# Performance work log

Measured on AMD Instinct MI355X. Metric: run time of the kernel, lower is better.

The kernel has to match this reference:

```python
import jax, jax.numpy as jnp
import numpy as np

N = 50_000        # nodes
E = 1_600_000     # edges (avg degree 32)
H = 64            # hidden_channels
DEPTH = 3         # -> 2*DEPTH mid conv layers


def setup_inputs() -> dict:
    key = jax.random.key(0)
    ks = jax.random.split(key, 8)
    x = jax.random.normal(ks[0], (N, 1), dtype=jnp.float32)
    edge_index = jax.random.randint(ks[1], (2, E), 0, N, dtype=jnp.int32)
    s = 0.1  # small init scale
    W_in = s * jax.random.normal(ks[2], (2 * 1 + 1, H), dtype=jnp.float32)
    b_in = jnp.zeros((H,), jnp.float32)
    W_mid = s * jax.random.normal(ks[3], (2 * DEPTH, 2 * H + 1, H), dtype=jnp.float32)
    b_mid = jnp.zeros((2 * DEPTH, H), jnp.float32)
    W_out = s * jax.random.normal(ks[4], (2 * H + 1, 1), dtype=jnp.float32)
    b_out = jnp.zeros((1,), jnp.float32)
    return {"x": x, "edge_index": edge_index, "W_in": W_in, "b_in": b_in,
            "W_mid": W_mid, "b_mid": b_mid, "W_out": W_out, "b_out": b_out}


def _conv(x, src, dst, sign, inv_deg, W, b):
    """Directional_EdgeConv: mean_{j->i} Linear([x_i, x_j - x_i, sign(j-i)])."""
    x_i = x[dst]                                   # [E, F] target feats
    x_j = x[src]                                   # [E, F] source feats
    feat = jnp.concatenate([x_i, x_j - x_i, sign], axis=-1)  # [E, 2F+1]
    msg = feat @ W + b                             # [E, out]
    agg = jax.ops.segment_sum(msg, dst, num_segments=x.shape[0])  # [N, out]
    return agg * inv_deg                           # mean aggregation


def reference(x, edge_index, W_in, b_in, W_mid, b_mid, W_out, b_out):
    src = edge_index[0]
    dst = edge_index[1]
    # vectorized replacement of the per-edge Python sign loop
    sign = jnp.sign((src - dst).astype(x.dtype))[:, None]        # [E, 1]
    deg = jax.ops.segment_sum(jnp.ones((src.shape[0],), x.dtype), dst,
                              num_segments=x.shape[0])
    inv_deg = (1.0 / jnp.maximum(deg, 1.0))[:, None]             # [N, 1]

    x2 = _conv(x, src, dst, sign, inv_deg, W_in, b_in)
    for l in range(DEPTH):
        x1 = jax.nn.leaky_relu(
            _conv(x2, src, dst, sign, inv_deg, W_mid[2 * l], b_mid[2 * l]))
        x2 = jax.nn.leaky_relu(
            _conv(x1, src, dst, sign, inv_deg, W_mid[2 * l + 1], b_mid[2 * l + 1]) + x2)
    return _conv(x2, src, dst, sign, inv_deg, W_out, b_out) + x
```

## Files before the change

kernel.cpp:

```cpp
#include <hip/hip_runtime.h>
#include <hip/hip_fp16.h>

#define HDIM 64
#define NEG_SLOPE 0.01f
#define CAPB 8192
#define BCAP 6144
#define EPB  4096

typedef _Float16 half8 __attribute__((ext_vector_type(8)));
typedef float f32x4 __attribute__((ext_vector_type(4)));

static __device__ __forceinline__ float h_lo(unsigned d) {
    return __half2float(__ushort_as_half((unsigned short)(d & 0xffffu)));
}
static __device__ __forceinline__ float h_hi(unsigned d) {
    return __half2float(__ushort_as_half((unsigned short)(d >> 16)));
}
static __device__ __forceinline__ unsigned packh(float a, float b) {
    unsigned short ra = __half_as_ushort(__float2half(a));
    unsigned short rb = __half_as_ushort(__float2half(b));
    return ((unsigned)rb << 16) | (unsigned)ra;
}
static __device__ __forceinline__ half8 u4h(uint4 v) {
    union { uint4 u; half8 h; } x; x.u = v; return x.h;
}
static __device__ __forceinline__ __half2 uh2(unsigned u) {
    union { unsigned u; __half2 h; } x; x.u = u; return x.h;
}

__global__ void k_setup(int ptotal, const float* __restrict__ W_mid,
                        unsigned short* __restrict__ WTh,
                        int NB, int* gcur, int N, unsigned* xAP, unsigned* xBP,
                        float* tvec) {
    int i = blockIdx.x * blockDim.x + threadIdx.x;
    if (i < ptotal) {
        int l = i >> 13;
        int rem = i & 8191;
        int h = rem >> 7;
        int k = rem & 127;
        const float* W = W_mid + (size_t)l * 129 * 64;
        float v = W[k * 64 + h] - ((k < 64) ? W[(64 + k) * 64 + h] : 0.f);
        WTh[i] = __half_as_ushort(__float2half(v));
    }
    if (i < NB) gcur[i] = i * CAPB;
    if (i < 32) xAP[(size_t)N * 32 + i] = 0u;
    else if (i < 64) xBP[(size_t)N * 32 + (i - 32)] = 0u;
    else if (i == 64) tvec[N] = 0.f;
}

__global__ __launch_bounds__(1024) void k_bucket(
        int E, const int* __restrict__ src, const int* __restrict__ dst,
        int* gcur, unsigned* __restrict__ bucketed, int NB) {
    __shared__ int lh[512];
    __shared__ int sd[512];
    __shared__ int lbase[512];
    __shared__ unsigned sorted[EPB];
    int t = threadIdx.x;
    int e0 = blockIdx.x * EPB;
    if (t < 512) lh[t] = 0;
    __syncthreads();
    int dv[4], sv[4], rv[4];
#pragma unroll
    for (int k = 0; k < 4; ++k) {
        int e = e0 + k * 1024 + t;
        dv[k] = (e < E) ? dst[e] : -1;
        sv[k] = (e < E) ? src[e] : 0;
    }
#pragma unroll
    for (int k = 0; k < 4; ++k)
        rv[k] = (dv[k] >= 0) ? atomicAdd(&lh[((unsigned)dv[k]) >> 7], 1) : 0;
    __syncthreads();
    int c = (t < 512) ? lh[t] : 0;
    if (t < 512) {
        lbase[t] = (c > 0) ? atomicAdd(&gcur[t], c) : 0;
        sd[t] = c;
    }
    __syncthreads();
    int x = c;
    for (int s = 1; s < 512; s <<= 1) {
        int p = (t < 512 && t >= s) ? sd[t - s] : 0;
        __syncthreads();
        if (t < 512) { x += p; sd[t] = x; }
        __syncthreads();
    }
#pragma unroll
    for (int k = 0; k < 4; ++k) {
        if (dv[k] >= 0) {
            int b = ((unsigned)dv[k]) >> 7;
            sorted[sd[b] - lh[b] + rv[k]] = ((unsigned)dv[k] << 16) | (unsigned)sv[k];
        }
    }
    __syncthreads();
    int ntot = sd[511];
    for (int i = t; i < ntot; i += 1024) {
        unsigned w = sorted[i];
        int b = (int)(w >> 23);
        int pos = lbase[b] + (i - (sd[b] - lh[b]));
        if (pos < (b + 1) * CAPB) bucketed[pos] = w;
    }
}

__global__ __launch_bounds__(512) void k_csr(
        int N, int NB, const unsigned* __restrict__ bucketed, const int* __restrict__ gcur,
        unsigned short* __restrict__ csr, unsigned short* __restrict__ pcsr,
        int* __restrict__ rowptr, float* __restrict__ ssinv,
        const float* __restrict__ x0, const float* __restrict__ W_in,
        const float* __restrict__ b_in, unsigned* __restrict__ xAP) {
    __shared__ unsigned st[BCAP];
    __shared__ unsigned short lpcsr[128 * 64];
    __shared__ int hist[128], cur[128], excl[128], sgp[128], sdegl[128];
    __shared__ float sssl[128];
    __shared__ int gsd[512];
    int b = blockIdx.x, t = threadIdx.x;
    int n0 = b << 7;
    int nn = min(128, N - n0);
    int cc = (t < NB) ? min(gcur[t] - t * CAPB, CAPB) : 0;
    gsd[t] = cc;
    __syncthreads();
    int xs = cc;
    for (int s = 1; s < 512; s <<= 1) {
        int p = (t >= s) ? gsd[t - s] : 0;
        __syncthreads();
        xs += p;
        gsd[t] = xs;
        __syncthreads();
    }
    int cnt = min(gcur[b] - b * CAPB, CAPB);
    int base = gsd[b] - cnt;
    if (b == NB - 1 && t == 0) rowptr[N] = gsd[NB - 1];
    if (t < 128) { hist[t] = 0; sgp[t] = 0; }
    unsigned sent = ((unsigned)N << 16) | (unsigned)N;
    for (int i = t; i < 4096; i += 512) ((unsigned*)lpcsr)[i] = sent;
    __syncthreads();
    bool single = (cnt <= BCAP);
    for (int off = 0; off < cnt; off += BCAP) {
        int bs = min(BCAP, cnt - off);
        for (int i = t; i < bs; i += 512) {
            unsigned w = bucketed[b * CAPB + off + i];
            if (single) st[i] = w;
            int d = (int)(w >> 16);
            int s = (int)(w & 0xffffu);
            int dl = d - n0;
            atomicAdd(&hist[dl], 1);
            atomicAdd(&sgp[dl], ((s < d) ? 1024 : 0) + ((s == d) ? 1 : 0));
        }
    }
    __syncthreads();
    int deg_t = (t < 128) ? hist[t] : 0;
    int x = deg_t;
    for (int s = 1; s < 128; s <<= 1) {
        int p = (t < 128 && t >= s) ? hist[t - s] : 0;
        __syncthreads();
        if (t < 128) { x += p; hist[t] = x; }
        __syncthreads();
    }
    if (t < 128) {
        int ex = hist[t] - deg_t;
        excl[t] = ex;
        cur[t] = ex;
        sdegl[t] = deg_t;
        float ssv = 0.f;
        if (t < nn) {
            rowptr[n0 + t] = base + ex;
            int sg = sgp[t];
            int lt = sg >> 10, eq = sg & 1023;
            float ss = (float)(deg_t - eq - 2 * lt);
            ssv = (deg_t > 0) ? ss / (float)deg_t : 0.f;
            ssinv[n0 + t] = ssv;
        }
        sssl[t] = ssv;
    }
    __syncthreads();
    for (int off = 0; off < cnt; off += BCAP) {
        int bs = min(BCAP, cnt - off);
        if (!single) {
            for (int i = t; i < bs; i += 512) st[i] = bucketed[b * CAPB + off + i];
            __syncthreads();
        }
        for (int i = t; i < bs; i += 512) {
            unsigned w = st[i];
            int dl = (int)(w >> 16) - n0;
            unsigned short sval = (unsigned short)(w & 0xffffu);
            int p = atomicAdd(&cur[dl], 1);
            csr[base + p] = sval;
            int r = p - excl[dl];
            if (r < 64) lpcsr[(dl << 6) + r] = sval;
        }
        if (!single) __syncthreads();
    }
    __syncthreads();
    {
        uint4* gp = (uint4*)(pcsr + ((size_t)b << 13));
        const uint4* lp = (const uint4*)lpcsr;
        for (int i = t; i < 1024; i += 512) gp[i] = lp[i];
    }
    int lane = t & 63;
    int wvq = t >> 6;
    float w1 = W_in[lane], w2 = W_in[64 + lane], w3 = W_in[128 + lane];
    float bi = b_in[lane];
    for (int i = 0; i < 16; ++i) {
        int nd = (wvq << 4) + i;
        int node = n0 + nd;
        if (node >= N) break;
        int deg = sdegl[nd];
        float s;
        if (deg <= 64) {
            int sl = (int)lpcsr[(nd << 6) + lane];
            s = (sl < N) ? x0[sl] : 0.f;
        } else {
            s = 0.f;
            int bg = base + excl[nd], en = bg + deg;
            for (int e = bg + lane; e < en; e += 64) s += x0[csr[e]];
        }
        for (int m = 32; m >= 1; m >>= 1) s += __shfl_xor(s, m, 64);
        float invd = 1.f / (float)max(deg, 1);
        float mean = s * invd;
        float xi = x0[node];
        float y = xi * (w1 - w2) + mean * w2 + sssl[nd] * w3 + bi;
        if (deg == 0) y = 0.f;
        float ylo = __shfl(y, (2 * lane) & 63, 64);
        float yhi = __shfl(y, (2 * lane + 1) & 63, 64);
        if (lane < 32) xAP[(size_t)node * 32 + lane] = packh(ylo, yhi);
    }
}

static __device__ __forceinline__ void chunk_acc(
        const uint4* __restrict__ xin16, int sv, int base, int sub, int lq,
        __half2& c0, __half2& c1, __half2& c2, __half2& c3) {
    int s0 = __shfl(sv, base + sub, 64);
    int s1 = __shfl(sv, base + 8 + sub, 64);
    int s2 = __shfl(sv, base + 16 + sub, 64);
    int s3 = __shfl(sv, base + 24 + sub, 64);
    uint4 d0 = xin16[(size_t)s0 * 8 + lq];
    uint4 d1 = xin16[(size_t)s1 * 8 + lq];
    uint4 d2 = xin16[(size_t)s2 * 8 + lq];
    uint4 d3 = xin16[(size_t)s3 * 8 + lq];
    c0 = __hadd2(c0, __hadd2(__hadd2(uh2(d0.x), uh2(d1.x)), __hadd2(uh2(d2.x), uh2(d3.x))));
    c1 = __hadd2(c1, __hadd2(__hadd2(uh2(d0.y), uh2(d1.y)), __hadd2(uh2(d2.y), uh2(d3.y))));
    c2 = __hadd2(c2, __hadd2(__hadd2(uh2(d0.z), uh2(d1.z)), __hadd2(uh2(d2.z), uh2(d3.z))));
    c3 = __hadd2(c3, __hadd2(__hadd2(uh2(d0.w), uh2(d1.w)), __hadd2(uh2(d2.w), uh2(d3.w))));
}

static __device__ __forceinline__ void slow_gather(
        const uint4* __restrict__ xin16, const unsigned short* __restrict__ csr,
        int beg, int end, int N, int lane, int sub, int lq, float* a) {
#pragma unroll
    for (int j = 0; j < 8; ++j) a[j] = 0.f;
    for (int tb = beg; tb < end; tb += 64) {
        int cnt = min(64, end - tb);
        int sv = (lane < cnt) ? (int)csr[tb + lane] : N;
        int ng = (cnt + 7) >> 3;
        for (int g = 0; g < ng; ++g) {
            int si = __shfl(sv, (g << 3) + sub, 64);
            uint4 d = xin16[(size_t)si * 8 + lq];
            a[0] += h_lo(d.x); a[1] += h_hi(d.x);
            a[2] += h_lo(d.y); a[3] += h_hi(d.y);
            a[4] += h_lo(d.z); a[5] += h_hi(d.z);
            a[6] += h_lo(d.w); a[7] += h_hi(d.w);
        }
    }
#pragma unroll
    for (int m = 8; m <= 32; m <<= 1) {
#pragma unroll
        for (int j = 0; j < 8; ++j) a[j] += __shfl_xor(a[j], m, 64);
    }
}

template <bool RES, bool TOUT>
__global__ __launch_bounds__(256) void k_layer(
        int N, const unsigned* __restrict__ xinP,
        const unsigned* __restrict__ xresP, unsigned* __restrict__ xoutP,
        const int* __restrict__ rowptr, const unsigned short* __restrict__ csr,
        const unsigned short* __restrict__ pcsr,
        const float* __restrict__ ssinv,
        const unsigned short* __restrict__ WThl,
        const float* __restrict__ W3, const float* __restrict__ bias,
        const float* __restrict__ Wt, float* __restrict__ tvec) {
    __shared__ unsigned Ald[16 * 64];
    __shared__ float Cld[16 * 64];
    __shared__ int sdeg[16];
    __shared__ float sss[16];

    int t = threadIdx.x;
    int lane = t & 63;
    int wv = t >> 6;
    int n0 = blockIdx.x << 4;
    int kg = lane >> 4;

    int cb = (wv << 4) + (lane & 15);
    const uint4* wp = (const uint4*)WThl;
    uint4 b0 = wp[cb * 16 + kg + 0];
    uint4 b1 = wp[cb * 16 + kg + 4];
    uint4 b2 = wp[cb * 16 + kg + 8];
    uint4 b3 = wp[cb * 16 + kg + 12];

    const uint4* xin16 = (const uint4*)xinP;
    int sub = lane >> 3;
    int lq = lane & 7;
    int ndb = wv << 2;

    int svp[4];
#pragma unroll
    for (int q = 0; q < 4; ++q)
        svp[q] = (int)pcsr[((size_t)(n0 + ndb + q) << 6) + lane];

#pragma unroll
    for (int qp = 0; qp < 2; ++qp) {
        int ndA = ndb + (qp << 1);
        int ndB = ndA + 1;
        int nodeA = n0 + ndA, nodeB = n0 + ndB;
        int ncA = min(nodeA, N - 1), ncB = min(nodeB, N - 1);
        int begA = __builtin_amdgcn_readfirstlane(rowptr[ncA]);
        int endA = __builtin_amdgcn_readfirstlane(rowptr[ncA + 1]);
        int begB = __builtin_amdgcn_readfirstlane(rowptr[ncB]);
        int endB = __builtin_amdgcn_readfirstlane(rowptr[ncB + 1]);
        int degA = (nodeA < N) ? (endA - begA) : 0;
        int degB = (nodeB < N) ? (endB - begB) : 0;
        float ssvA = ssinv[ncA];
        float ssvB = ssinv[ncB];
        uint4 xiA = make_uint4(0u, 0u, 0u, 0u), xiB = make_uint4(0u, 0u, 0u, 0u);
        if (lane < 8) {
            if (nodeA < N) xiA = xin16[(size_t)ncA * 8 + lane];
            if (nodeB < N) xiB = xin16[(size_t)ncB * 8 + lane];
        }
        uint4 mvA, mvB;
        if (max(degA, degB) <= 64) {
            __half2 z = uh2(0u);
            __half2 cA0 = z, cA1 = z, cA2 = z, cA3 = z;
            __half2 cB0 = z, cB1 = z, cB2 = z, cB3 = z;
            int svA = svp[qp << 1], svB = svp[(qp << 1) + 1];
            chunk_acc(xin16, svA, 0, sub, lq, cA0, cA1, cA2, cA3);
            chunk_acc(xin16, svB, 0, sub, lq, cB0, cB1, cB2, cB3);
            if (degA > 32) chunk_acc(xin16, svA, 32, sub, lq, cA0, cA1, cA2, cA3);
            if (degB > 32) chunk_acc(xin16, svB, 32, sub, lq, cB0, cB1, cB2, cB3);
#pragma unroll
            for (int m = 8; m <= 32; m <<= 1) {
                cA0 = __hadd2(cA0, uh2((unsigned)__shfl_xor((int)*(unsigned*)&cA0, m, 64)));
                cA1 = __hadd2(cA1, uh2((unsigned)__shfl_xor((int)*(unsigned*)&cA1, m, 64)));
                cA2 = __hadd2(cA2, uh2((unsigned)__shfl_xor((int)*(unsigned*)&cA2, m, 64)));
                cA3 = __hadd2(cA3, uh2((unsigned)__shfl_xor((int)*(unsigned*)&cA3, m, 64)));
                cB0 = __hadd2(cB0, uh2((unsigned)__shfl_xor((int)*(unsigned*)&cB0, m, 64)));
                cB1 = __hadd2(cB1, uh2((unsigned)__shfl_xor((int)*(unsigned*)&cB1, m, 64)));
                cB2 = __hadd2(cB2, uh2((unsigned)__shfl_xor((int)*(unsigned*)&cB2, m, 64)));
                cB3 = __hadd2(cB3, uh2((unsigned)__shfl_xor((int)*(unsigned*)&cB3, m, 64)));
            }
            float idA = 1.f / (float)max(degA, 1);
            float idB = 1.f / (float)max(degB, 1);
            mvA.x = packh(__half2float(__low2half(cA0)) * idA, __half2float(__high2half(cA0)) * idA);
            mvA.y = packh(__half2float(__low2half(cA1)) * idA, __half2float(__high2half(cA1)) * idA);
            mvA.z = packh(__half2float(__low2half(cA2)) * idA, __half2float(__high2half(cA2)) * idA);
            mvA.w = packh(__half2float(__low2half(cA3)) * idA, __half2float(__high2half(cA3)) * idA);
            mvB.x = packh(__half2float(__low2half(cB0)) * idB, __half2float(__high2half(cB0)) * idB);
            mvB.y = packh(__half2float(__low2half(cB1)) * idB, __half2float(__high2half(cB1)) * idB);
            mvB.z = packh(__half2float(__low2half(cB2)) * idB, __half2float(__high2half(cB2)) * idB);
            mvB.w = packh(__half2float(__low2half(cB3)) * idB, __half2float(__high2half(cB3)) * idB);
        } else {
            float aA[8], aB[8];
            slow_gather(xin16, csr, begA, endA, N, lane, sub, lq, aA);
            slow_gather(xin16, csr, begB, endB, N, lane, sub, lq, aB);
            float idA = 1.f / (float)max(degA, 1);
            float idB = 1.f / (float)max(degB, 1);
            mvA.x = packh(aA[0] * idA, aA[1] * idA);
            mvA.y = packh(aA[2] * idA, aA[3] * idA);
            mvA.z = packh(aA[4] * idA, aA[5] * idA);
            mvA.w = packh(aA[6] * idA, aA[7] * idA);
            mvB.x = packh(aB[0] * idB, aB[1] * idB);
            mvB.y = packh(aB[2] * idB, aB[3] * idB);
            mvB.z = packh(aB[4] * idB, aB[5] * idB);
            mvB.w = packh(aB[6] * idB, aB[7] * idB);
        }
        if (lane < 8) {
            int gxA = lane ^ (ndA & 7), gmA = (8 + lane) ^ (ndA & 7);
            int gxB = lane ^ (ndB & 7), gmB = (8 + lane) ^ (ndB & 7);
            ((uint4*)Ald)[ndA * 16 + gxA] = xiA;
            ((uint4*)Ald)[ndA * 16 + gmA] = mvA;
            ((uint4*)Ald)[ndB * 16 + gxB] = xiB;
            ((uint4*)Ald)[ndB * 16 + gmB] = mvB;
        }
        if (lane == 0) {
            sdeg[ndA] = degA; sss[ndA] = ssvA;
            sdeg[ndB] = degB; sss[ndB] = ssvB;
        }
    }
    __syncthreads();

    int r = lane & 15;
    const uint4* ap = (const uint4*)Ald;
    int rx = (r & 7);
    uint4 fa0 = ap[r * 16 + ((0 + kg) ^ rx)];
    uint4 fa1 = ap[r * 16 + ((4 + kg) ^ rx)];
    uint4 fa2 = ap[r * 16 + ((8 + kg) ^ rx)];
    uint4 fa3 = ap[r * 16 + ((12 + kg) ^ rx)];
    f32x4 acc = {0.f, 0.f, 0.f, 0.f};
    acc = __builtin_amdgcn_mfma_f32_16x16x32_f16(u4h(fa0), u4h(b0), acc, 0, 0, 0);
    acc = __builtin_amdgcn_mfma_f32_16x16x32_f16(u4h(fa1), u4h(b1), acc, 0, 0, 0);
    acc = __builtin_amdgcn_mfma_f32_16x16x32_f16(u4h(fa2), u4h(b2), acc, 0, 0, 0);
    acc = __builtin_amdgcn_mfma_f32_16x16x32_f16(u4h(fa3), u4h(b3), acc, 0, 0, 0);
#pragma unroll
    for (int reg = 0; reg < 4; ++reg)
        Cld[(kg * 4 + reg) * 64 + (wv << 4) + r] = acc[reg];
    __syncthreads();

    int nd = t >> 4;
    int node = n0 + nd;
    if (node < N) {
        int dg = sdeg[nd];
        float ss = sss[nd];
        float tp = 0.f;
#pragma unroll
        for (int jj = 0; jj < 2; ++jj) {
            int j = (t & 15) + jj * 16;
            float y0 = Cld[nd * 64 + 2 * j];
            float y1 = Cld[nd * 64 + 2 * j + 1];
            float2 w3 = ((const float2*)W3)[j];
            float2 bb = ((const float2*)bias)[j];
            y0 += ss * w3.x + bb.x;
            y1 += ss * w3.y + bb.y;
            if (dg == 0) { y0 = 0.f; y1 = 0.f; }
            if (RES) {
                unsigned rw = xresP[(size_t)node * 32 + j];
                y0 += h_lo(rw);
                y1 += h_hi(rw);
            }
            y0 = (y0 > 0.f) ? y0 : NEG_SLOPE * y0;
            y1 = (y1 > 0.f) ? y1 : NEG_SLOPE * y1;
            if (TOUT) {
                float2 wt = ((const float2*)Wt)[j];
                tp += y0 * wt.x + y1 * wt.y;
            }
            xoutP[(size_t)node * 32 + j] = packh(y0, y1);
        }
        if (TOUT) {
            tp += __shfl_xor(tp, 1, 64);
            tp += __shfl_xor(tp, 2, 64);
            tp += __shfl_xor(tp, 4, 64);
            tp += __shfl_xor(tp, 8, 64);
            if ((t & 15) == 0) tvec[node] = tp;
        }
    }
}

__global__ void k_out(int N, const unsigned* __restrict__ xAP, const float* __restrict__ x0,
                      const int* __restrict__ rowptr, const unsigned short* __restrict__ csr,
                      const unsigned short* __restrict__ pcsr,
                      const float* __restrict__ ssinv, const float* __restrict__ t,
                      const float* __restrict__ W_out, const float* __restrict__ b_out,
                      float* __restrict__ out) {
    int wid = blockIdx.x * (blockDim.x >> 6) + (threadIdx.x >> 6);
    int lane = threadIdx.x & 63;
    if (wid >= N) return;
    int beg = rowptr[wid], end = rowptr[wid + 1];
    int deg = end - beg;
    float s;
    if (deg <= 64) {
        int sl = (int)pcsr[((size_t)wid << 6) + lane];
        s = t[sl];
    } else {
        s = 0.f;
        for (int e = beg + lane; e < end; e += 64) s += t[csr[e]];
    }
    unsigned xw = xAP[(size_t)wid * 32 + (lane >> 1)];
    float xf = (lane & 1) ? h_hi(xw) : h_lo(xw);
    float p = xf * (W_out[lane] - W_out[64 + lane]);
    for (int m = 32; m >= 1; m >>= 1) {
        s += __shfl_xor(s, m, 64);
        p += __shfl_xor(p, m, 64);
    }
    float invd = 1.f / (float)max(deg, 1);
    float y = p + s * invd + ssinv[wid] * W_out[128] + b_out[0];
    if (deg == 0) y = 0.f;
    if (lane == 0) out[wid] = y + x0[wid];
}

static inline size_t align16(size_t x) { return (x + 15) & ~(size_t)15; }

extern "C" void kernel_launch(void* const* d_in, const int* in_sizes, int n_in,
                              void* d_out, int out_size, void* d_ws, size_t ws_size,
                              hipStream_t stream) {
    const float* x0    = (const float*)d_in[0];
    const int*   ei    = (const int*)d_in[1];
    const float* W_in  = (const float*)d_in[2];
    const float* b_in  = (const float*)d_in[3];
    const float* W_mid = (const float*)d_in[4];
    const float* b_mid = (const float*)d_in[5];
    const float* W_out = (const float*)d_in[6];
    const float* b_out = (const float*)d_in[7];
    float* out = (float*)d_out;

    const int N = in_sizes[0];
    const int E = in_sizes[1] / 2;
    const int L = in_sizes[4] / (129 * 64);
    const int NB = (N + 127) >> 7;
    const int* src = ei;
    const int* dst = ei + E;

    char* p = (char*)d_ws;
    unsigned short* WTh = (unsigned short*)p; p += align16((size_t)L * 64 * 128 * 2);
    unsigned* xAP = (unsigned*)p; p += align16((size_t)(N + 1) * 32 * 4);
    unsigned* xBP = (unsigned*)p; p += align16((size_t)(N + 1) * 32 * 4);
    unsigned* bucketed = (unsigned*)p; p += align16((size_t)NB * CAPB * 4);
    unsigned short* csr = (unsigned short*)p; p += align16((size_t)E * 2);
    unsigned short* pcsr = (unsigned short*)p; p += align16((size_t)NB * 8192 * 2);
    int* gcur          = (int*)p; p += align16((size_t)(NB + 1) * 4);
    int* rowptr        = (int*)p; p += align16((size_t)(N + 1) * 4);
    float* ssinv       = (float*)p; p += align16((size_t)N * 4);
    float* t           = (float*)p; p += align16((size_t)(N + 1) * 4);

    const int nb_w4 = (N + 3) / 4;
    const int nb_bkt = (E + EPB - 1) / EPB;
    const int ptotal = L * 64 * 128;
    const int nb_lay = (N + 15) / 16;

    k_setup<<<(ptotal + 255) / 256, 256, 0, stream>>>(ptotal, W_mid, WTh, NB, gcur, N, xAP, xBP, t);
    k_bucket<<<nb_bkt, 1024, 0, stream>>>(E, src, dst, gcur, bucketed, NB);
    k_csr<<<NB, 512, 0, stream>>>(N, NB, bucketed, gcur, csr, pcsr, rowptr, ssinv,
                                  x0, W_in, b_in, xAP);

    for (int l = 0; l < L / 2; ++l) {
        bool last = (l == L / 2 - 1);
        const unsigned short* Wa = WTh + (size_t)(2 * l) * 64 * 128;
        const unsigned short* Wb = WTh + (size_t)(2 * l + 1) * 64 * 128;
        const float* W3a = W_mid + (size_t)(2 * l) * 129 * 64 + 128 * 64;
        const float* W3b = W_mid + (size_t)(2 * l + 1) * 129 * 64 + 128 * 64;

        k_layer<false, false><<<nb_lay, 256, 0, stream>>>(
            N, xAP, nullptr, xBP, rowptr, csr, pcsr, ssinv,
            Wa, W3a, b_mid + (size_t)(2 * l) * HDIM, nullptr, nullptr);
        if (!last) {
            k_layer<true, false><<<nb_lay, 256, 0, stream>>>(
                N, xBP, xAP, xAP, rowptr, csr, pcsr, ssinv,
                Wb, W3b, b_mid + (size_t)(2 * l + 1) * HDIM, nullptr, nullptr);
        } else {
            k_layer<true, true><<<nb_lay, 256, 0, stream>>>(
                N, xBP, xAP, xAP, rowptr, csr, pcsr, ssinv,
                Wb, W3b, b_mid + (size_t)(2 * l + 1) * HDIM, W_out + 64, t);
        }
    }

    k_out<<<nb_w4, 256, 0, stream>>>(N, xAP, x0, rowptr, csr, pcsr, ssinv, t,
                                     W_out, b_out, out);
}
```

Baseline: 234.5 us.

## Stage first neighbor chunk of all four nodes into LDS via global_load_lds

The first 32 neighbor rows for each of the wave's four nodes are now loaded asynchronously straight into LDS (64 KB of shared staging per block) through global_load_lds, all issued before a single vmcnt wait. Previously the gather ran one pair of nodes at a time through registers. The aim is more memory-level parallelism on the random gathers. The cost is a large LDS footprint that limits occupancy to a couple of blocks per CU, plus an extra LDS round trip.

```diff
diff --git a/kernel.cpp b/kernel.cpp
--- a/kernel.cpp
+++ b/kernel.cpp
@@ -26,6 +26,11 @@
 }
 static __device__ __forceinline__ __half2 uh2(unsigned u) {
     union { unsigned u; __half2 h; } x; x.u = u; return x.h;
+}
+static __device__ __forceinline__ void dma16(const unsigned* gsrc, unsigned* ldst) {
+    __builtin_amdgcn_global_load_lds(
+        (const __attribute__((address_space(1))) unsigned*)gsrc,
+        (__attribute__((address_space(3))) unsigned*)ldst, 16, 0, 0);
 }
 
 __global__ void k_setup(int ptotal, const float* __restrict__ W_mid,
@@ -276,6 +281,7 @@
         const unsigned short* __restrict__ WThl,
         const float* __restrict__ W3, const float* __restrict__ bias,
         const float* __restrict__ Wt, float* __restrict__ tvec) {
+    __shared__ unsigned stage[16 * 1024];
     __shared__ unsigned Ald[16 * 64];
     __shared__ float Cld[16 * 64];
     __shared__ int sdeg[16];
@@ -299,88 +305,88 @@
     int lq = lane & 7;
     int ndb = wv << 2;
 
-    int svp[4];
-#pragma unroll
-    for (int q = 0; q < 4; ++q)
-        svp[q] = (int)pcsr[((size_t)(n0 + ndb + q) << 6) + lane];
-
-#pragma unroll
-    for (int qp = 0; qp < 2; ++qp) {
-        int ndA = ndb + (qp << 1);
-        int ndB = ndA + 1;
-        int nodeA = n0 + ndA, nodeB = n0 + ndB;
-        int ncA = min(nodeA, N - 1), ncB = min(nodeB, N - 1);
-        int begA = __builtin_amdgcn_readfirstlane(rowptr[ncA]);
-        int endA = __builtin_amdgcn_readfirstlane(rowptr[ncA + 1]);
-        int begB = __builtin_amdgcn_readfirstlane(rowptr[ncB]);
-        int endB = __builtin_amdgcn_readfirstlane(rowptr[ncB + 1]);
-        int degA = (nodeA < N) ? (endA - begA) : 0;
-        int degB = (nodeB < N) ? (endB - begB) : 0;
-        float ssvA = ssinv[ncA];
-        float ssvB = ssinv[ncB];
-        uint4 xiA = make_uint4(0u, 0u, 0u, 0u), xiB = make_uint4(0u, 0u, 0u, 0u);
+    int svp[4], degq[4], begq[4], endq[4];
+    float ssq[4];
+#pragma unroll
+    for (int q = 0; q < 4; ++q) {
+        int node = n0 + ndb + q;
+        int nc = min(node, N - 1);
+        svp[q] = (int)pcsr[((size_t)node << 6) + lane];
+        int bg = __builtin_amdgcn_readfirstlane(rowptr[nc]);
+        int en = __builtin_amdgcn_readfirstlane(rowptr[nc + 1]);
+        begq[q] = bg; endq[q] = en;
+        degq[q] = (node < N) ? (en - bg) : 0;
+        ssq[q] = ssinv[nc];
+    }
+
+#pragma unroll
+    for (int q = 0; q < 4; ++q) {
+        int sv = svp[q];
+        unsigned* sb = &stage[(ndb + q) << 10];
+#pragma unroll
+        for (int g = 0; g < 4; ++g) {
+            int sidx = __shfl(sv, (g << 3) + sub, 64);
+            const unsigned* gsrc = xinP + ((size_t)sidx << 5) + (lq << 2);
+            dma16(gsrc, sb + (g << 8));
+        }
+    }
+    uint4 xi[4];
+#pragma unroll
+    for (int q = 0; q < 4; ++q) {
+        int node = n0 + ndb + q;
+        xi[q] = make_uint4(0u, 0u, 0u, 0u);
+        if (lane < 8 && node < N) xi[q] = xin16[(size_t)min(node, N - 1) * 8 + lane];
+    }
+    asm volatile("s_waitcnt vmcnt(0)" ::: "memory");
+    __builtin_amdgcn_sched_barrier(0);
+
+    uint4 mv[4];
+#pragma unroll
+    for (int q = 0; q < 4; ++q) {
+        if (degq[q] <= 64) {
+            const uint4* sp = (const uint4*)&stage[(ndb + q) << 10];
+            uint4 d0 = sp[(sub) * 8 + lq];
+            uint4 d1 = sp[(sub + 8) * 8 + lq];
+            uint4 d2 = sp[(sub + 16) * 8 + lq];
+            uint4 d3 = sp[(sub + 24) * 8 + lq];
+            __half2 c0 = __hadd2(__hadd2(uh2(d0.x), uh2(d1.x)), __hadd2(uh2(d2.x), uh2(d3.x)));
+            __half2 c1 = __hadd2(__hadd2(uh2(d0.y), uh2(d1.y)), __hadd2(uh2(d2.y), uh2(d3.y)));
+            __half2 c2 = __hadd2(__hadd2(uh2(d0.z), uh2(d1.z)), __hadd2(uh2(d2.z), uh2(d3.z)));
+            __half2 c3 = __hadd2(__hadd2(uh2(d0.w), uh2(d1.w)), __hadd2(uh2(d2.w), uh2(d3.w)));
+            if (degq[q] > 32) chunk_acc(xin16, svp[q], 32, sub, lq, c0, c1, c2, c3);
+#pragma unroll
+            for (int m = 8; m <= 32; m <<= 1) {
+                c0 = __hadd2(c0, uh2((unsigned)__shfl_xor((int)*(unsigned*)&c0, m, 64)));
+                c1 = __hadd2(c1, uh2((unsigned)__shfl_xor((int)*(unsigned*)&c1, m, 64)));
+                c2 = __hadd2(c2, uh2((unsigned)__shfl_xor((int)*(unsigned*)&c2, m, 64)));
+                c3 = __hadd2(c3, uh2((unsigned)__shfl_xor((int)*(unsigned*)&c3, m, 64)));
+            }
+            float id = 1.f / (float)max(degq[q], 1);
+            mv[q].x = packh(__half2float(__low2half(c0)) * id, __half2float(__high2half(c0)) * id);
+            mv[q].y = packh(__half2float(__low2half(c1)) * id, __half2float(__high2half(c1)) * id);
+            mv[q].z = packh(__half2float(__low2half(c2)) * id, __half2float(__high2half(c2)) * id);
+            mv[q].w = packh(__half2float(__low2half(c3)) * id, __half2float(__high2half(c3)) * id);
+        } else {
+            float a[8];
+            slow_gather(xin16, csr, begq[q], endq[q], N, lane, sub, lq, a);
+            float id = 1.f / (float)degq[q];
+            mv[q].x = packh(a[0] * id, a[1] * id);
+            mv[q].y = packh(a[2] * id, a[3] * id);
+            mv[q].z = packh(a[4] * id, a[5] * id);
+            mv[q].w = packh(a[6] * id, a[7] * id);
+        }
+    }
+
+#pragma unroll
+    for (int q = 0; q < 4; ++q) {
+        int nd = ndb + q;
         if (lane < 8) {
-            if (nodeA < N) xiA = xin16[(size_t)ncA * 8 + lane];
-            if (nodeB < N) xiB = xin16[(size_t)ncB * 8 + lane];
-        }
-        uint4 mvA, mvB;
-        if (max(degA, degB) <= 64) {
-            __half2 z = uh2(0u);
-            __half2 cA0 = z, cA1 = z, cA2 = z, cA3 = z;
-            __half2 cB0 = z, cB1 = z, cB2 = z, cB3 = z;
-            int svA = svp[qp << 1], svB = svp[(qp << 1) + 1];
-            chunk_acc(xin16, svA, 0, sub, lq, cA0, cA1, cA2, cA3);
-            chunk_acc(xin16, svB, 0, sub, lq, cB0, cB1, cB2, cB3);
-            if (degA > 32) chunk_acc(xin16, svA, 32, sub, lq, cA0, cA1, cA2, cA3);
-            if (degB > 32) chunk_acc(xin16, svB, 32, sub, lq, cB0, cB1, cB2, cB3);
-#pragma unroll
-            for (int m = 8; m <= 32; m <<= 1) {
-                cA0 = __hadd2(cA0, uh2((unsigned)__shfl_xor((int)*(unsigned*)&cA0, m, 64)));
-                cA1 = __hadd2(cA1, uh2((unsigned)__shfl_xor((int)*(unsigned*)&cA1, m, 64)));
-                cA2 = __hadd2(cA2, uh2((unsigned)__shfl_xor((int)*(unsigned*)&cA2, m, 64)));
-                cA3 = __hadd2(cA3, uh2((unsigned)__shfl_xor((int)*(unsigned*)&cA3, m, 64)));
-                cB0 = __hadd2(cB0, uh2((unsigned)__shfl_xor((int)*(unsigned*)&cB0, m, 64)));
-                cB1 = __hadd2(cB1, uh2((unsigned)__shfl_xor((int)*(unsigned*)&cB1, m, 64)));
-                cB2 = __hadd2(cB2, uh2((unsigned)__shfl_xor((int)*(unsigned*)&cB2, m, 64)));
-                cB3 = __hadd2(cB3, uh2((unsigned)__shfl_xor((int)*(unsigned*)&cB3, m, 64)));
-            }
-            float idA = 1.f / (float)max(degA, 1);
-            float idB = 1.f / (float)max(degB, 1);
-            mvA.x = packh(__half2float(__low2half(cA0)) * idA, __half2float(__high2half(cA0)) * idA);
-            mvA.y = packh(__half2float(__low2half(cA1)) * idA, __half2float(__high2half(cA1)) * idA);
-            mvA.z = packh(__half2float(__low2half(cA2)) * idA, __half2float(__high2half(cA2)) * idA);
-            mvA.w = packh(__half2float(__low2half(cA3)) * idA, __half2float(__high2half(cA3)) * idA);
-            mvB.x = packh(__half2float(__low2half(cB0)) * idB, __half2float(__high2half(cB0)) * idB);
-            mvB.y = packh(__half2float(__low2half(cB1)) * idB, __half2float(__high2half(cB1)) * idB);
-            mvB.z = packh(__half2float(__low2half(cB2)) * idB, __half2float(__high2half(cB2)) * idB);
-            mvB.w = packh(__half2float(__low2half(cB3)) * idB, __half2float(__high2half(cB3)) * idB);
-        } else {
-            float aA[8], aB[8];
-            slow_gather(xin16, csr, begA, endA, N, lane, sub, lq, aA);
-            slow_gather(xin16, csr, begB, endB, N, lane, sub, lq, aB);
-            float idA = 1.f / (float)max(degA, 1);
-            float idB = 1.f / (float)max(degB, 1);
-            mvA.x = packh(aA[0] * idA, aA[1] * idA);
-            mvA.y = packh(aA[2] * idA, aA[3] * idA);
-            mvA.z = packh(aA[4] * idA, aA[5] * idA);
-            mvA.w = packh(aA[6] * idA, aA[7] * idA);
-            mvB.x = packh(aB[0] * idB, aB[1] * idB);
-            mvB.y = packh(aB[2] * idB, aB[3] * idB);
-            mvB.z = packh(aB[4] * idB, aB[5] * idB);
-            mvB.w = packh(aB[6] * idB, aB[7] * idB);
-        }
-        if (lane < 8) {
-            int gxA = lane ^ (ndA & 7), gmA = (8 + lane) ^ (ndA & 7);
-            int gxB = lane ^ (ndB & 7), gmB = (8 + lane) ^ (ndB & 7);
-            ((uint4*)Ald)[ndA * 16 + gxA] = xiA;
-            ((uint4*)Ald)[ndA * 16 + gmA] = mvA;
-            ((uint4*)Ald)[ndB * 16 + gxB] = xiB;
-            ((uint4*)Ald)[ndB * 16 + gmB] = mvB;
-        }
-        if (lane == 0) {
-            sdeg[ndA] = degA; sss[ndA] = ssvA;
-            sdeg[ndB] = degB; sss[ndB] = ssvB;
-        }
+            int gx = lane ^ (nd & 7);
+            int gm = (8 + lane) ^ (nd & 7);
+            ((uint4*)Ald)[nd * 16 + gx] = xi[q];
+            ((uint4*)Ald)[nd * 16 + gm] = mv[q];
+        }
+        if (lane == 0) { sdeg[nd] = degq[q]; sss[nd] = ssq[q]; }
     }
     __syncthreads();
 
```

After: 350.0 us. +49.3%, slower.
